# Kernel optimization log

Measured on AMD Instinct MI355X. Metric: run time of the kernel, lower is better.

Reference implementation:

```python
import jax, jax.numpy as jnp
import numpy as np

T, H, I, E, K = 16384, 2048, 1024, 8, 2  # tokens, hidden, intermediate, experts, top_k


def setup_inputs() -> dict:
    key = jax.random.key(0)
    k1, k2, k3, k4, k5 = jax.random.split(key, 5)
    hidden_states = jax.random.normal(k1, (T, H), dtype=jnp.float32)
    expert_routing_table = jax.random.randint(k2, (T, K), 0, E, dtype=jnp.int32)
    rw = jax.random.uniform(k3, (T, K), dtype=jnp.float32)
    router_weights = rw  # op consumes raw per-token gate weights
    # fused gate+up projection per expert: [E, 2I, H] (Linear-style [out, in])
    w13 = jax.random.normal(k4, (E, 2 * I, H), dtype=jnp.float32) * (1.0 / np.sqrt(H))
    # down projection per expert: [E, H, I]
    w2 = jax.random.normal(k5, (E, H, I), dtype=jnp.float32) * (1.0 / np.sqrt(I))
    return {
        "hidden_states": hidden_states,
        "expert_routing_table": expert_routing_table,
        "router_weights": router_weights,
        "w13": w13,
        "w2": w2,
    }


def reference(hidden_states, expert_routing_table, router_weights, w13, w2):
    # Faithful math of torch.ops.hpu.mixture_of_experts (silu activation):
    # for each token t and each routed expert e (top-k):
    #   g, u = split(x_t @ w13_e^T); y += router_w * ((silu(g) * u) @ w2_e^T)
    num_experts = w13.shape[0]
    out = jnp.zeros_like(hidden_states)
    for e in range(num_experts):  # small fixed expert loop
        # combine weight for expert e per token: sum over top-k slots routed to e
        coef = jnp.sum(
            jnp.where(expert_routing_table == e, router_weights, 0.0), axis=-1
        )  # [T]
        gu = hidden_states @ w13[e].T            # [T, 2I]
        g, u = jnp.split(gu, 2, axis=-1)         # SwiGLU halves
        act = jax.nn.silu(g) * u                 # [T, I]
        out = out + coef[:, None] * (act @ w2[e].T)  # [T, H]
    return out
```

## Files before the change

kernel.cpp:

```cpp
#include <hip/hip_runtime.h>
#include <hip/hip_bf16.h>
#include <stdint.h>

#define TOKS 16384
#define HDIM 2048
#define IDIM 1024
#define NEXP 8
#define TOPK 2
#define NPAIR (TOKS*TOPK)

typedef __attribute__((ext_vector_type(4))) float f32x4;
typedef __attribute__((ext_vector_type(8))) __bf16 bf16x8;
typedef __attribute__((ext_vector_type(8))) unsigned short u16x8;

#define GLOAD_LDS16(gp, lp) \
  __builtin_amdgcn_global_load_lds((const __attribute__((address_space(1))) void*)(gp), \
                                   (__attribute__((address_space(3))) void*)(lp), 16, 0, 0)

#define LGKM_WAITN(n) asm volatile("s_waitcnt lgkmcnt(" #n ")" ::: "memory")
#define VM_WAITN(n)   asm volatile("s_waitcnt vmcnt(" #n ")" ::: "memory")
#define SBAR0()       __builtin_amdgcn_sched_barrier(0)

__device__ __forceinline__ unsigned short f2bf(float f) {
  unsigned int u = __float_as_uint(f);
  u += 0x7FFF + ((u >> 16) & 1);
  return (unsigned short)(u >> 16);
}
__device__ __forceinline__ float bf2f(unsigned short h) {
  return __uint_as_float(((unsigned int)h) << 16);
}

#define W13_N8 (NEXP * 2 * IDIM * HDIM / 8)
#define W2_N8  (NEXP * HDIM * IDIM / 8)
#define X_N8   (TOKS * HDIM / 8)
__global__ __launch_bounds__(256) void cvt_all(const float* __restrict__ w13,
                                               const float* __restrict__ w2,
                                               const float* __restrict__ x,
                                               unsigned short* __restrict__ w13b,
                                               unsigned short* __restrict__ w2b,
                                               unsigned short* __restrict__ xb) {
  int i = blockIdx.x * 256 + threadIdx.x;
  const float* s; unsigned short* d; int j;
  if (i < W13_N8)              { s = w13; d = w13b; j = i; }
  else if (i < W13_N8 + W2_N8) { s = w2;  d = w2b;  j = i - W13_N8; }
  else                         { s = x;   d = xb;   j = i - W13_N8 - W2_N8; }
  const float4* sp = (const float4*)s + (size_t)j * 2;
  float4 a = sp[0], b = sp[1];
  u16x8 o;
  o[0] = f2bf(a.x); o[1] = f2bf(a.y); o[2] = f2bf(a.z); o[3] = f2bf(a.w);
  o[4] = f2bf(b.x); o[5] = f2bf(b.y); o[6] = f2bf(b.z); o[7] = f2bf(b.w);
  *((u16x8*)d + j) = o;
}

__global__ void route_count(const int* __restrict__ ert, int* __restrict__ ctrl) {
  int p = blockIdx.x * 256 + threadIdx.x;
  if (p < NPAIR) atomicAdd(&ctrl[ert[p]], 1);
}

__global__ void route_scan(int* __restrict__ ctrl) {
  if (blockIdx.x == 0 && threadIdx.x == 0) {
    int off = 0;
    for (int e = 0; e < NEXP; ++e) { ctrl[8 + e] = off; ctrl[16 + e] = off; off += ctrl[e]; }
    int toff = 0;
    for (int e = 0; e < NEXP; ++e) { ctrl[24 + e] = toff; toff += (ctrl[e] + 255) >> 8; }
    ctrl[32] = toff;
  }
}

__global__ void route_scatter(const int* __restrict__ ert, const float* __restrict__ rw,
                              int* __restrict__ ctrl, int* __restrict__ porig,
                              float* __restrict__ pcoef, int* __restrict__ pinv) {
  int p = blockIdx.x * 256 + threadIdx.x;
  if (p < NPAIR) {
    int e = ert[p];
    int pos = atomicAdd(&ctrl[16 + e], 1);
    porig[pos] = p;
    pcoef[pos] = rw[p];
    pinv[p]    = pos;
  }
}


#define RD_SET(lb, A0v, A1v, B0v, B1v) do {                                          \
  _Pragma("unroll") for (int mi = 0; mi < 4; ++mi) {                                 \
    int r_ = wr * 128 + mi * 16 + l15;                                               \
    A0v[mi] = *(const bf16x8*)((lb) + r_ * 64 + ((l16 ^ ((r_ >> 1) & 3)) << 4)); }   \
  _Pragma("unroll") for (int ni = 0; ni < 2; ++ni) {                                 \
    int nb_ = wc * 64 + ni * 16 + l15;                                               \
    B0v[ni] = *(const bf16x8*)((lb) + 16384 + nb_ * 64 + ((l16 ^ ((nb_ >> 1) & 3)) << 4)); } \
  _Pragma("unroll") for (int ni = 0; ni < 2; ++ni) {                                 \
    int nb_ = wc * 64 + 32 + ni * 16 + l15;                                          \
    B1v[ni] = *(const bf16x8*)((lb) + 16384 + nb_ * 64 + ((l16 ^ ((nb_ >> 1) & 3)) << 4)); } \
  _Pragma("unroll") for (int mi = 0; mi < 4; ++mi) {                                 \
    int r_ = wr * 128 + 64 + mi * 16 + l15;                                          \
    A1v[mi] = *(const bf16x8*)((lb) + r_ * 64 + ((l16 ^ ((r_ >> 1) & 3)) << 4)); }   \
} while (0)

#define MMQ(qm, qn, Av, Bv) do {                                                     \
  __builtin_amdgcn_s_setprio(1);                                                     \
  _Pragma("unroll") for (int mi = 0; mi < 4; ++mi)                                   \
    _Pragma("unroll") for (int ni = 0; ni < 2; ++ni)                                 \
      acc[qm][qn][mi][ni] = __builtin_amdgcn_mfma_f32_16x16x32_bf16(                 \
          Av[mi], Bv[ni], acc[qm][qn][mi][ni], 0, 0, 0);                             \
  __builtin_amdgcn_s_setprio(0);                                                     \
} while (0)

#define ITER(i, cA0, cA1, cB0, cB1, nA0, nA1, nB0, nB1) do {                         \
  LGKM_WAITN(6);                                                                     \
  MMQ(0, 0, cA0, cB0);                                                               \
  LGKM_WAITN(4);                                                                     \
  MMQ(0, 1, cA0, cB1);                                                               \
  LGKM_WAITN(0);                                                                     \
  MMQ(1, 0, cA1, cB0);                                                               \
  if ((i) < NT - 1) {                                                                \
    VM_WAITN(0);                                                                     \
    __builtin_amdgcn_s_barrier();                                                    \
    SBAR0();                                                                         \
    if ((i) + 2 < NT) STAGE((i) + 2);                                                \
    RD_SET(lds + (((i) + 1) & 1) * 32768, nA0, nA1, nB0, nB1);                       \
    SBAR0();                                                                         \
  }                                                                                  \
  MMQ(1, 1, cA1, cB1);                                                               \
} while (0)

#define TILE_MAP()                                                                   \
  const int x_ = bid & 7, k_ = bid >> 3;                                             \
  const int cb = k_ & 7;                                                             \
  const int tile = ((k_ >> 3) << 3) + x_;

__global__ __launch_bounds__(512, 2) void gemm1(const unsigned short* __restrict__ xb,
                                                const unsigned short* __restrict__ w13b,
                                                const int* __restrict__ ctrl,
                                                const int* __restrict__ porig,
                                                unsigned short* __restrict__ actb) {
  __shared__ __align__(16) char lds[65536];
  const int bid  = blockIdx.x;
  TILE_MAP();
  if (tile >= ctrl[32]) return;
  int e = 7;
  #pragma unroll
  for (int k = 7; k >= 1; --k) if (tile < ctrl[24 + k]) e = k - 1;
  const int rb   = tile - ctrl[24 + e];
  const int Ne   = ctrl[e];
  const int base = ctrl[8 + e];
  const int row0 = rb * 256;
  const int c0   = cb * 128;
  const int tid  = threadIdx.x;
  const int wid  = tid >> 6;
  const int lane = tid & 63;
  const int wr   = wid >> 2;
  const int wc   = wid & 3;
  const int l15  = lane & 15;
  const int l16  = lane >> 4;
  const int NT   = HDIM / 32;

  const unsigned short *gA0, *gA1, *gB0, *gB1;
  {
    int rl = wid * 16 + (lane >> 2);
    int r0 = rl, r1 = 128 + rl;
    int c80 = (lane & 3) ^ ((r0 >> 1) & 3);
    int c81 = (lane & 3) ^ ((r1 >> 1) & 3);
    int rr0 = row0 + r0; if (rr0 > Ne - 1) rr0 = Ne - 1;
    int rr1 = row0 + r1; if (rr1 > Ne - 1) rr1 = Ne - 1;
    gA0 = xb + (size_t)(porig[base + rr0] >> 1) * HDIM + c80 * 8;
    gA1 = xb + (size_t)(porig[base + rr1] >> 1) * HDIM + c81 * 8;
    int g0 = ((r0 & 32) ? IDIM : 0) + c0 + ((r0 >> 6) << 5) + (r0 & 31);
    int g1 = ((r1 & 32) ? IDIM : 0) + c0 + ((r1 >> 6) << 5) + (r1 & 31);
    gB0 = w13b + ((size_t)e * (2 * IDIM) + g0) * HDIM + c80 * 8;
    gB1 = w13b + ((size_t)e * (2 * IDIM) + g1) * HDIM + c81 * 8;
  }

  f32x4 acc[2][2][4][2];
  #pragma unroll
  for (int qm = 0; qm < 2; ++qm)
    #pragma unroll
    for (int qn = 0; qn < 2; ++qn)
      #pragma unroll
      for (int mi = 0; mi < 4; ++mi)
        #pragma unroll
        for (int ni = 0; ni < 2; ++ni) acc[qm][qn][mi][ni] = (f32x4)(0.0f);

  auto STAGE = [&](int kt) {
    char* d = lds + (kt & 1) * 32768 + wid * 1024;
    GLOAD_LDS16(gA0 + kt * 32, d);
    GLOAD_LDS16(gA1 + kt * 32, d + 8192);
    GLOAD_LDS16(gB0 + kt * 32, d + 16384);
    GLOAD_LDS16(gB1 + kt * 32, d + 24576);
  };

  bf16x8 A0a[4], A1a[4], B0a[2], B1a[2];
  bf16x8 A0b[4], A1b[4], B0b[2], B1b[2];

  STAGE(0); STAGE(1);
  VM_WAITN(4);
  __builtin_amdgcn_s_barrier();
  SBAR0();
  RD_SET(lds, A0a, A1a, B0a, B1a);
  SBAR0();

  for (int i = 0; i < NT; i += 2) {
    ITER(i,     A0a, A1a, B0a, B1a, A0b, A1b, B0b, B1b);
    ITER(i + 1, A0b, A1b, B0b, B1b, A0a, A1a, B0a, B1a);
  }

  #pragma unroll
  for (int qm = 0; qm < 2; ++qm)
    #pragma unroll
    for (int mi = 0; mi < 4; ++mi)
      #pragma unroll
      for (int jj = 0; jj < 4; ++jj) {
        int r = wr * 128 + qm * 64 + mi * 16 + l16 * 4 + jj;
        int rr = row0 + r;
        if (rr < Ne) {
          #pragma unroll
          for (int ni = 0; ni < 2; ++ni) {
            float g = acc[qm][0][mi][ni][jj];
            float u = acc[qm][1][mi][ni][jj];
            float a = g / (1.0f + __expf(-g)) * u;
            actb[(size_t)(base + rr) * IDIM + (c0 + wc * 32 + ni * 16 + l15)] = f2bf(a);
          }
        }
      }
}

__global__ __launch_bounds__(512, 2) void gemm2(const unsigned short* __restrict__ actb,
                                                const unsigned short* __restrict__ w2b,
                                                const int* __restrict__ ctrl,
                                                const float* __restrict__ pcoef,
                                                unsigned short* __restrict__ yb) {
  __shared__ __align__(16) char lds[65536];
  const int bid  = blockIdx.x;
  TILE_MAP();
  if (tile >= ctrl[32]) return;
  int e = 7;
  #pragma unroll
  for (int k = 7; k >= 1; --k) if (tile < ctrl[24 + k]) e = k - 1;
  const int rb   = tile - ctrl[24 + e];
  const int Ne   = ctrl[e];
  const int base = ctrl[8 + e];
  const int row0 = rb * 256;
  const int n0   = cb * 256;
  const int tid  = threadIdx.x;
  const int wid  = tid >> 6;
  const int lane = tid & 63;
  const int wr   = wid >> 2;
  const int wc   = wid & 3;
  const int l15  = lane & 15;
  const int l16  = lane >> 4;
  const int NT   = IDIM / 32;

  const unsigned short *gA0, *gA1, *gB0, *gB1;
  {
    int rl = wid * 16 + (lane >> 2);
    int r0 = rl, r1 = 128 + rl;
    int c80 = (lane & 3) ^ ((r0 >> 1) & 3);
    int c81 = (lane & 3) ^ ((r1 >> 1) & 3);
    int rr0 = row0 + r0; if (rr0 > Ne - 1) rr0 = Ne - 1;
    int rr1 = row0 + r1; if (rr1 > Ne - 1) rr1 = Ne - 1;
    gA0 = actb + (size_t)(base + rr0) * IDIM + c80 * 8;
    gA1 = actb + (size_t)(base + rr1) * IDIM + c81 * 8;
    gB0 = w2b + ((size_t)e * HDIM + n0 + r0) * IDIM + c80 * 8;
    gB1 = w2b + ((size_t)e * HDIM + n0 + r1) * IDIM + c81 * 8;
  }

  f32x4 acc[2][2][4][2];
  #pragma unroll
  for (int qm = 0; qm < 2; ++qm)
    #pragma unroll
    for (int qn = 0; qn < 2; ++qn)
      #pragma unroll
      for (int mi = 0; mi < 4; ++mi)
        #pragma unroll
        for (int ni = 0; ni < 2; ++ni) acc[qm][qn][mi][ni] = (f32x4)(0.0f);

  auto STAGE = [&](int kt) {
    char* d = lds + (kt & 1) * 32768 + wid * 1024;
    GLOAD_LDS16(gA0 + kt * 32, d);
    GLOAD_LDS16(gA1 + kt * 32, d + 8192);
    GLOAD_LDS16(gB0 + kt * 32, d + 16384);
    GLOAD_LDS16(gB1 + kt * 32, d + 24576);
  };

  bf16x8 A0a[4], A1a[4], B0a[2], B1a[2];
  bf16x8 A0b[4], A1b[4], B0b[2], B1b[2];

  STAGE(0); STAGE(1);
  VM_WAITN(4);
  __builtin_amdgcn_s_barrier();
  SBAR0();
  RD_SET(lds, A0a, A1a, B0a, B1a);
  SBAR0();

  for (int i = 0; i < NT; i += 2) {
    ITER(i,     A0a, A1a, B0a, B1a, A0b, A1b, B0b, B1b);
    ITER(i + 1, A0b, A1b, B0b, B1b, A0a, A1a, B0a, B1a);
  }

  #pragma unroll
  for (int qm = 0; qm < 2; ++qm)
    #pragma unroll
    for (int mi = 0; mi < 4; ++mi)
      #pragma unroll
      for (int jj = 0; jj < 4; ++jj) {
        int r = wr * 128 + qm * 64 + mi * 16 + l16 * 4 + jj;
        int rr = row0 + r;
        if (rr < Ne) {
          float cf = pcoef[base + rr];
          #pragma unroll
          for (int qn = 0; qn < 2; ++qn)
            #pragma unroll
            for (int ni = 0; ni < 2; ++ni) {
              int col = n0 + wc * 64 + qn * 32 + ni * 16 + l15;
              yb[(size_t)(base + rr) * HDIM + col] = f2bf(acc[qm][qn][mi][ni][jj] * cf);
            }
        }
      }
}

__global__ __launch_bounds__(256) void reduce2(const unsigned short* __restrict__ yb,
                                               const int* __restrict__ pinv,
                                               float* __restrict__ out) {
  int i = blockIdx.x * 256 + threadIdx.x;
  int t = i >> 8;
  int g = i & 255;
  int p0 = pinv[2 * t], p1 = pinv[2 * t + 1];
  u16x8 a = *((const u16x8*)(yb + (size_t)p0 * HDIM) + g);
  u16x8 b = *((const u16x8*)(yb + (size_t)p1 * HDIM) + g);
  float4 o0, o1;
  o0.x = bf2f(a[0]) + bf2f(b[0]); o0.y = bf2f(a[1]) + bf2f(b[1]);
  o0.z = bf2f(a[2]) + bf2f(b[2]); o0.w = bf2f(a[3]) + bf2f(b[3]);
  o1.x = bf2f(a[4]) + bf2f(b[4]); o1.y = bf2f(a[5]) + bf2f(b[5]);
  o1.z = bf2f(a[6]) + bf2f(b[6]); o1.w = bf2f(a[7]) + bf2f(b[7]);
  float4* dst = (float4*)(out + (size_t)t * HDIM) + g * 2;
  dst[0] = o0; dst[1] = o1;
}

extern "C" void kernel_launch(void* const* d_in, const int* in_sizes, int n_in,
                              void* d_out, int out_size, void* d_ws, size_t ws_size,
                              hipStream_t stream) {
  const float* x   = (const float*)d_in[0];
  const int*   ert = (const int*)d_in[1];
  const float* rw  = (const float*)d_in[2];
  const float* w13 = (const float*)d_in[3];
  const float* w2  = (const float*)d_in[4];
  float* out = (float*)d_out;

  char* ws = (char*)d_ws;
  size_t off = 0;
  auto alloc = [&](size_t bytes) { char* p = ws + off; off += (bytes + 255) & ~255ULL; return p; };
  int*            ctrl  = (int*)           alloc(256);
  int*            porig = (int*)           alloc((size_t)NPAIR * 4);
  float*          pcoef = (float*)         alloc((size_t)NPAIR * 4);
  int*            pinv  = (int*)           alloc((size_t)NPAIR * 4);
  unsigned short* w2b   = (unsigned short*)alloc((size_t)NEXP * HDIM * IDIM * 2);
  unsigned short* actb  = (unsigned short*)alloc((size_t)NPAIR * IDIM * 2);
  unsigned short* w13b  = (unsigned short*)alloc((size_t)NEXP * 2 * IDIM * HDIM * 2);
  unsigned short* xb    = (unsigned short*)alloc((size_t)TOKS * HDIM * 2);
  unsigned short* yb    = w13b;

  hipMemsetAsync(ctrl, 0, 256, stream);

  cvt_all<<<(W13_N8 + W2_N8 + X_N8) / 256, 256, 0, stream>>>(w13, w2, x, w13b, w2b, xb);

  route_count  <<<NPAIR / 256, 256, 0, stream>>>(ert, ctrl);
  route_scan   <<<1, 64, 0, stream>>>(ctrl);
  route_scatter<<<NPAIR / 256, 256, 0, stream>>>(ert, rw, ctrl, porig, pcoef, pinv);

  gemm1<<<136 * 8, 512, 0, stream>>>(xb, w13b, ctrl, porig, actb);
  gemm2<<<136 * 8, 512, 0, stream>>>(actb, w2b, ctrl, pcoef, yb);
  reduce2<<<(TOKS * HDIM / 8) / 256, 256, 0, stream>>>(yb, pinv, out);
}
```

Baseline: 863.7 us.

## Shrink GEMM tiles to 256x128 and simplify pipeline to single-stage register reads

Halves the N dimension of each block tile in both expert GEMMs (256x256 to 256x128 in gemm1's gate/up pair, 256x128 in gemm2), doubling the grid to 2176 blocks and cutting LDS to 48KB. The unrolled ping-pong register double-buffering with staggered LDS waits is replaced by a simpler loop that reads all fragments, waits for LDS, then issues 16 MFMAs per wave. The aim is more blocks for load balance and occupancy, at the cost of lower arithmetic intensity per tile and less overlap of LDS reads with MFMA.

```diff
diff --git a/kernel.cpp b/kernel.cpp
--- a/kernel.cpp
+++ b/kernel.cpp
@@ -81,80 +81,72 @@
 }
 
 
-#define RD_SET(lb, A0v, A1v, B0v, B1v) do {                                          \
+#define RD8(lb) do {                                                                 \
   _Pragma("unroll") for (int mi = 0; mi < 4; ++mi) {                                 \
-    int r_ = wr * 128 + mi * 16 + l15;                                               \
-    A0v[mi] = *(const bf16x8*)((lb) + r_ * 64 + ((l16 ^ ((r_ >> 1) & 3)) << 4)); }   \
-  _Pragma("unroll") for (int ni = 0; ni < 2; ++ni) {                                 \
+    int r_ = wr * 64 + mi * 16 + l15;                                                \
+    fA[mi] = *(const bf16x8*)((lb) + r_ * 64 + ((l16 ^ ((r_ >> 1) & 3)) << 4)); }    \
+  _Pragma("unroll") for (int ni = 0; ni < 4; ++ni) {                                 \
     int nb_ = wc * 64 + ni * 16 + l15;                                               \
-    B0v[ni] = *(const bf16x8*)((lb) + 16384 + nb_ * 64 + ((l16 ^ ((nb_ >> 1) & 3)) << 4)); } \
-  _Pragma("unroll") for (int ni = 0; ni < 2; ++ni) {                                 \
-    int nb_ = wc * 64 + 32 + ni * 16 + l15;                                          \
-    B1v[ni] = *(const bf16x8*)((lb) + 16384 + nb_ * 64 + ((l16 ^ ((nb_ >> 1) & 3)) << 4)); } \
-  _Pragma("unroll") for (int mi = 0; mi < 4; ++mi) {                                 \
-    int r_ = wr * 128 + 64 + mi * 16 + l15;                                          \
-    A1v[mi] = *(const bf16x8*)((lb) + r_ * 64 + ((l16 ^ ((r_ >> 1) & 3)) << 4)); }   \
+    fB[ni] = *(const bf16x8*)((lb) + 16384 + nb_ * 64 + ((l16 ^ ((nb_ >> 1) & 3)) << 4)); } \
 } while (0)
 
-#define MMQ(qm, qn, Av, Bv) do {                                                     \
+#define MFMA16() do {                                                                \
   __builtin_amdgcn_s_setprio(1);                                                     \
   _Pragma("unroll") for (int mi = 0; mi < 4; ++mi)                                   \
-    _Pragma("unroll") for (int ni = 0; ni < 2; ++ni)                                 \
-      acc[qm][qn][mi][ni] = __builtin_amdgcn_mfma_f32_16x16x32_bf16(                 \
-          Av[mi], Bv[ni], acc[qm][qn][mi][ni], 0, 0, 0);                             \
+    _Pragma("unroll") for (int ni = 0; ni < 4; ++ni)                                 \
+      acc[mi][ni] = __builtin_amdgcn_mfma_f32_16x16x32_bf16(                         \
+          fA[mi], fB[ni], acc[mi][ni], 0, 0, 0);                                     \
   __builtin_amdgcn_s_setprio(0);                                                     \
 } while (0)
 
-#define ITER(i, cA0, cA1, cB0, cB1, nA0, nA1, nB0, nB1) do {                         \
-  LGKM_WAITN(6);                                                                     \
-  MMQ(0, 0, cA0, cB0);                                                               \
-  LGKM_WAITN(4);                                                                     \
-  MMQ(0, 1, cA0, cB1);                                                               \
-  LGKM_WAITN(0);                                                                     \
-  MMQ(1, 0, cA1, cB0);                                                               \
-  if ((i) < NT - 1) {                                                                \
-    VM_WAITN(0);                                                                     \
-    __builtin_amdgcn_s_barrier();                                                    \
-    SBAR0();                                                                         \
-    if ((i) + 2 < NT) STAGE((i) + 2);                                                \
-    RD_SET(lds + (((i) + 1) & 1) * 32768, nA0, nA1, nB0, nB1);                       \
-    SBAR0();                                                                         \
+#define GEMM_LOOP() do {                                                             \
+  STAGE(0);                                                                          \
+  VM_WAITN(0);                                                                       \
+  __builtin_amdgcn_s_barrier();                                                      \
+  for (int i = 0; i < NT; ++i) {                                                     \
+    if (i + 1 < NT) STAGE(i + 1);                                                    \
+    const char* lb_ = lds + (i & 1) * 24576;                                         \
+    RD8(lb_);                                                                        \
+    LGKM_WAITN(0); SBAR0();                                                          \
+    MFMA16();                                                                        \
+    if (i + 1 < NT) {                                                                \
+      VM_WAITN(0);                                                                   \
+      __builtin_amdgcn_s_barrier();                                                  \
+    }                                                                                \
   }                                                                                  \
-  MMQ(1, 1, cA1, cB1);                                                               \
 } while (0)
 
-#define TILE_MAP()                                                                   \
+#define TILE_MAP16()                                                                 \
   const int x_ = bid & 7, k_ = bid >> 3;                                             \
-  const int cb = k_ & 7;                                                             \
-  const int tile = ((k_ >> 3) << 3) + x_;
+  const int cb = k_ & 15;                                                            \
+  const int tile = ((k_ >> 4) << 3) + x_;
 
 __global__ __launch_bounds__(512, 2) void gemm1(const unsigned short* __restrict__ xb,
                                                 const unsigned short* __restrict__ w13b,
                                                 const int* __restrict__ ctrl,
                                                 const int* __restrict__ porig,
                                                 unsigned short* __restrict__ actb) {
-  __shared__ __align__(16) char lds[65536];
+  __shared__ __align__(16) char lds[49152];
   const int bid  = blockIdx.x;
-  TILE_MAP();
+  TILE_MAP16();
   if (tile >= ctrl[32]) return;
   int e = 7;
   #pragma unroll
   for (int k = 7; k >= 1; --k) if (tile < ctrl[24 + k]) e = k - 1;
-  const int rb   = tile - ctrl[24 + e];
   const int Ne   = ctrl[e];
   const int base = ctrl[8 + e];
-  const int row0 = rb * 256;
-  const int c0   = cb * 128;
+  const int row0 = (tile - ctrl[24 + e]) * 256;
+  const int c0   = cb * 64;
   const int tid  = threadIdx.x;
   const int wid  = tid >> 6;
   const int lane = tid & 63;
-  const int wr   = wid >> 2;
-  const int wc   = wid & 3;
+  const int wr   = wid >> 1;
+  const int wc   = wid & 1;
   const int l15  = lane & 15;
   const int l16  = lane >> 4;
   const int NT   = HDIM / 32;
 
-  const unsigned short *gA0, *gA1, *gB0, *gB1;
+  const unsigned short *gA0, *gA1, *gB0;
   {
     int rl = wid * 16 + (lane >> 2);
     int r0 = rl, r1 = 128 + rl;
@@ -164,63 +156,43 @@
     int rr1 = row0 + r1; if (rr1 > Ne - 1) rr1 = Ne - 1;
     gA0 = xb + (size_t)(porig[base + rr0] >> 1) * HDIM + c80 * 8;
     gA1 = xb + (size_t)(porig[base + rr1] >> 1) * HDIM + c81 * 8;
-    int g0 = ((r0 & 32) ? IDIM : 0) + c0 + ((r0 >> 6) << 5) + (r0 & 31);
-    int g1 = ((r1 & 32) ? IDIM : 0) + c0 + ((r1 >> 6) << 5) + (r1 & 31);
-    gB0 = w13b + ((size_t)e * (2 * IDIM) + g0) * HDIM + c80 * 8;
-    gB1 = w13b + ((size_t)e * (2 * IDIM) + g1) * HDIM + c81 * 8;
+    int n  = rl & 63;
+    int gr = ((n & 32) ? IDIM : 0) + c0 + ((rl >> 6) << 5) + (n & 31);
+    gB0 = w13b + ((size_t)e * (2 * IDIM) + gr) * HDIM + c80 * 8;
   }
 
-  f32x4 acc[2][2][4][2];
-  #pragma unroll
-  for (int qm = 0; qm < 2; ++qm)
+  f32x4 acc[4][4];
+  #pragma unroll
+  for (int mi = 0; mi < 4; ++mi)
     #pragma unroll
-    for (int qn = 0; qn < 2; ++qn)
-      #pragma unroll
-      for (int mi = 0; mi < 4; ++mi)
-        #pragma unroll
-        for (int ni = 0; ni < 2; ++ni) acc[qm][qn][mi][ni] = (f32x4)(0.0f);
+    for (int ni = 0; ni < 4; ++ni) acc[mi][ni] = (f32x4)(0.0f);
 
   auto STAGE = [&](int kt) {
-    char* d = lds + (kt & 1) * 32768 + wid * 1024;
+    char* d = lds + (kt & 1) * 24576 + wid * 1024;
     GLOAD_LDS16(gA0 + kt * 32, d);
     GLOAD_LDS16(gA1 + kt * 32, d + 8192);
     GLOAD_LDS16(gB0 + kt * 32, d + 16384);
-    GLOAD_LDS16(gB1 + kt * 32, d + 24576);
   };
 
-  bf16x8 A0a[4], A1a[4], B0a[2], B1a[2];
-  bf16x8 A0b[4], A1b[4], B0b[2], B1b[2];
-
-  STAGE(0); STAGE(1);
-  VM_WAITN(4);
-  __builtin_amdgcn_s_barrier();
-  SBAR0();
-  RD_SET(lds, A0a, A1a, B0a, B1a);
-  SBAR0();
-
-  for (int i = 0; i < NT; i += 2) {
-    ITER(i,     A0a, A1a, B0a, B1a, A0b, A1b, B0b, B1b);
-    ITER(i + 1, A0b, A1b, B0b, B1b, A0a, A1a, B0a, B1a);
-  }
-
-  #pragma unroll
-  for (int qm = 0; qm < 2; ++qm)
+  bf16x8 fA[4], fB[4];
+  GEMM_LOOP();
+
+  #pragma unroll
+  for (int mi = 0; mi < 4; ++mi)
     #pragma unroll
-    for (int mi = 0; mi < 4; ++mi)
-      #pragma unroll
-      for (int jj = 0; jj < 4; ++jj) {
-        int r = wr * 128 + qm * 64 + mi * 16 + l16 * 4 + jj;
-        int rr = row0 + r;
-        if (rr < Ne) {
-          #pragma unroll
-          for (int ni = 0; ni < 2; ++ni) {
-            float g = acc[qm][0][mi][ni][jj];
-            float u = acc[qm][1][mi][ni][jj];
-            float a = g / (1.0f + __expf(-g)) * u;
-            actb[(size_t)(base + rr) * IDIM + (c0 + wc * 32 + ni * 16 + l15)] = f2bf(a);
-          }
+    for (int jj = 0; jj < 4; ++jj) {
+      int r  = wr * 64 + mi * 16 + l16 * 4 + jj;
+      int rr = row0 + r;
+      if (rr < Ne) {
+        #pragma unroll
+        for (int ni = 0; ni < 2; ++ni) {
+          float g = acc[mi][ni][jj];
+          float u = acc[mi][ni + 2][jj];
+          float a = g / (1.0f + __expf(-g)) * u;
+          actb[(size_t)(base + rr) * IDIM + (c0 + wc * 32 + ni * 16 + l15)] = f2bf(a);
         }
       }
+    }
 }
 
 __global__ __launch_bounds__(512, 2) void gemm2(const unsigned short* __restrict__ actb,
@@ -228,28 +200,27 @@
                                                 const int* __restrict__ ctrl,
                                                 const float* __restrict__ pcoef,
                                                 unsigned short* __restrict__ yb) {
-  __shared__ __align__(16) char lds[65536];
+  __shared__ __align__(16) char lds[49152];
   const int bid  = blockIdx.x;
-  TILE_MAP();
+  TILE_MAP16();
   if (tile >= ctrl[32]) return;
   int e = 7;
   #pragma unroll
   for (int k = 7; k >= 1; --k) if (tile < ctrl[24 + k]) e = k - 1;
-  const int rb   = tile - ctrl[24 + e];
   const int Ne   = ctrl[e];
   const int base = ctrl[8 + e];
-  const int row0 = rb * 256;
-  const int n0   = cb * 256;
+  const int row0 = (tile - ctrl[24 + e]) * 256;
+  const int n0   = cb * 128;
   const int tid  = threadIdx.x;
   const int wid  = tid >> 6;
   const int lane = tid & 63;
-  const int wr   = wid >> 2;
-  const int wc   = wid & 3;
+  const int wr   = wid >> 1;
+  const int wc   = wid & 1;
   const int l15  = lane & 15;
   const int l16  = lane >> 4;
   const int NT   = IDIM / 32;
 
-  const unsigned short *gA0, *gA1, *gB0, *gB1;
+  const unsigned short *gA0, *gA1, *gB0;
   {
     int rl = wid * 16 + (lane >> 2);
     int r0 = rl, r1 = 128 + rl;
@@ -259,62 +230,40 @@
     int rr1 = row0 + r1; if (rr1 > Ne - 1) rr1 = Ne - 1;
     gA0 = actb + (size_t)(base + rr0) * IDIM + c80 * 8;
     gA1 = actb + (size_t)(base + rr1) * IDIM + c81 * 8;
-    gB0 = w2b + ((size_t)e * HDIM + n0 + r0) * IDIM + c80 * 8;
-    gB1 = w2b + ((size_t)e * HDIM + n0 + r1) * IDIM + c81 * 8;
+    gB0 = w2b + ((size_t)e * HDIM + n0 + rl) * IDIM + c80 * 8;
   }
 
-  f32x4 acc[2][2][4][2];
-  #pragma unroll
-  for (int qm = 0; qm < 2; ++qm)
+  f32x4 acc[4][4];
+  #pragma unroll
+  for (int mi = 0; mi < 4; ++mi)
     #pragma unroll
-    for (int qn = 0; qn < 2; ++qn)
-      #pragma unroll
-      for (int mi = 0; mi < 4; ++mi)
-        #pragma unroll
-        for (int ni = 0; ni < 2; ++ni) acc[qm][qn][mi][ni] = (f32x4)(0.0f);
+    for (int ni = 0; ni < 4; ++ni) acc[mi][ni] = (f32x4)(0.0f);
 
   auto STAGE = [&](int kt) {
-    char* d = lds + (kt & 1) * 32768 + wid * 1024;
+    char* d = lds + (kt & 1) * 24576 + wid * 1024;
     GLOAD_LDS16(gA0 + kt * 32, d);
     GLOAD_LDS16(gA1 + kt * 32, d + 8192);
     GLOAD_LDS16(gB0 + kt * 32, d + 16384);
-    GLOAD_LDS16(gB1 + kt * 32, d + 24576);
   };
 
-  bf16x8 A0a[4], A1a[4], B0a[2], B1a[2];
-  bf16x8 A0b[4], A1b[4], B0b[2], B1b[2];
-
-  STAGE(0); STAGE(1);
-  VM_WAITN(4);
-  __builtin_amdgcn_s_barrier();
-  SBAR0();
-  RD_SET(lds, A0a, A1a, B0a, B1a);
-  SBAR0();
-
-  for (int i = 0; i < NT; i += 2) {
-    ITER(i,     A0a, A1a, B0a, B1a, A0b, A1b, B0b, B1b);
-    ITER(i + 1, A0b, A1b, B0b, B1b, A0a, A1a, B0a, B1a);
-  }
-
-  #pragma unroll
-  for (int qm = 0; qm < 2; ++qm)
+  bf16x8 fA[4], fB[4];
+  GEMM_LOOP();
+
+  #pragma unroll
+  for (int mi = 0; mi < 4; ++mi)
     #pragma unroll
-    for (int mi = 0; mi < 4; ++mi)
-      #pragma unroll
-      for (int jj = 0; jj < 4; ++jj) {
-        int r = wr * 128 + qm * 64 + mi * 16 + l16 * 4 + jj;
-        int rr = row0 + r;
-        if (rr < Ne) {
-          float cf = pcoef[base + rr];
-          #pragma unroll
-          for (int qn = 0; qn < 2; ++qn)
-            #pragma unroll
-            for (int ni = 0; ni < 2; ++ni) {
-              int col = n0 + wc * 64 + qn * 32 + ni * 16 + l15;
-              yb[(size_t)(base + rr) * HDIM + col] = f2bf(acc[qm][qn][mi][ni][jj] * cf);
-            }
+    for (int jj = 0; jj < 4; ++jj) {
+      int r  = wr * 64 + mi * 16 + l16 * 4 + jj;
+      int rr = row0 + r;
+      if (rr < Ne) {
+        float cf = pcoef[base + rr];
+        #pragma unroll
+        for (int ni = 0; ni < 4; ++ni) {
+          int col = n0 + wc * 64 + ni * 16 + l15;
+          yb[(size_t)(base + rr) * HDIM + col] = f2bf(acc[mi][ni][jj] * cf);
         }
       }
+    }
 }
 
 __global__ __launch_bounds__(256) void reduce2(const unsigned short* __restrict__ yb,
@@ -366,7 +315,7 @@
   route_scan   <<<1, 64, 0, stream>>>(ctrl);
   route_scatter<<<NPAIR / 256, 256, 0, stream>>>(ert, rw, ctrl, porig, pcoef, pinv);
 
-  gemm1<<<136 * 8, 512, 0, stream>>>(xb, w13b, ctrl, porig, actb);
-  gemm2<<<136 * 8, 512, 0, stream>>>(actb, w2b, ctrl, pcoef, yb);
+  gemm1<<<2176, 512, 0, stream>>>(xb, w13b, ctrl, porig, actb);
+  gemm2<<<2176, 512, 0, stream>>>(actb, w2b, ctrl, pcoef, yb);
   reduce2<<<(TOKS * HDIM / 8) / 256, 256, 0, stream>>>(yb, pinv, out);
 }
```

After: 847.5 us. No clear change (-1.9%).

## Load B operand directly from global into registers and deepen A LDS pipeline

Applied to the files above, without the earlier changes.

Both MoE GEMM kernels stop staging the weight (B) tiles through LDS. Each wave now loads its B fragments straight from global memory into registers one k-step ahead. The freed LDS is used to turn the A-tile double buffer into a 4-stage ring prefetched three steps ahead, with vmcnt waits adjusted to match. The aim is to cut LDS traffic and bank pressure and to deepen latency hiding. The cost is more uncoalesced global loads per wave, duplicate B loads across the two wave rows, and more register pressure.

```diff
diff --git a/kernel.cpp b/kernel.cpp
--- a/kernel.cpp
+++ b/kernel.cpp
@@ -81,19 +81,20 @@
 }
 
 
-#define RD_SET(lb, A0v, A1v, B0v, B1v) do {                                          \
+#define RD_A(lb, A0v, A1v) do {                                                      \
   _Pragma("unroll") for (int mi = 0; mi < 4; ++mi) {                                 \
     int r_ = wr * 128 + mi * 16 + l15;                                               \
     A0v[mi] = *(const bf16x8*)((lb) + r_ * 64 + ((l16 ^ ((r_ >> 1) & 3)) << 4)); }   \
-  _Pragma("unroll") for (int ni = 0; ni < 2; ++ni) {                                 \
-    int nb_ = wc * 64 + ni * 16 + l15;                                               \
-    B0v[ni] = *(const bf16x8*)((lb) + 16384 + nb_ * 64 + ((l16 ^ ((nb_ >> 1) & 3)) << 4)); } \
-  _Pragma("unroll") for (int ni = 0; ni < 2; ++ni) {                                 \
-    int nb_ = wc * 64 + 32 + ni * 16 + l15;                                          \
-    B1v[ni] = *(const bf16x8*)((lb) + 16384 + nb_ * 64 + ((l16 ^ ((nb_ >> 1) & 3)) << 4)); } \
   _Pragma("unroll") for (int mi = 0; mi < 4; ++mi) {                                 \
     int r_ = wr * 128 + 64 + mi * 16 + l15;                                          \
     A1v[mi] = *(const bf16x8*)((lb) + r_ * 64 + ((l16 ^ ((r_ >> 1) & 3)) << 4)); }   \
+} while (0)
+
+#define LOADB(i, B) do {                                                             \
+  B[0][0] = *(const bf16x8*)(gB00 + (size_t)(i) * 32);                               \
+  B[0][1] = *(const bf16x8*)(gB01 + (size_t)(i) * 32);                               \
+  B[1][0] = *(const bf16x8*)(gB10 + (size_t)(i) * 32);                               \
+  B[1][1] = *(const bf16x8*)(gB11 + (size_t)(i) * 32);                               \
 } while (0)
 
 #define MMQ(qm, qn, Av, Bv) do {                                                     \
@@ -105,22 +106,39 @@
   __builtin_amdgcn_s_setprio(0);                                                     \
 } while (0)
 
-#define ITER(i, cA0, cA1, cB0, cB1, nA0, nA1, nB0, nB1) do {                         \
-  LGKM_WAITN(6);                                                                     \
-  MMQ(0, 0, cA0, cB0);                                                               \
-  LGKM_WAITN(4);                                                                     \
-  MMQ(0, 1, cA0, cB1);                                                               \
-  LGKM_WAITN(0);                                                                     \
-  MMQ(1, 0, cA1, cB0);                                                               \
+#define ITER(i, cA0, cA1, cB, nA0, nA1, nB) do {                                     \
+  if ((i) + 3 < NT) STAGE((i) + 3);                                                  \
+  if ((i) + 1 < NT) LOADB((i) + 1, nB);                                              \
+  if ((i) < NT - 3)      { VM_WAITN(6); }                                            \
+  else if ((i) < NT - 1) { VM_WAITN(4); }                                            \
+  else                   { VM_WAITN(0); }                                            \
+  SBAR0();                                                                           \
+  LGKM_WAITN(4); SBAR0();                                                            \
+  MMQ(0, 0, cA0, (cB)[0]);                                                           \
+  MMQ(0, 1, cA0, (cB)[1]);                                                           \
+  LGKM_WAITN(0); SBAR0();                                                            \
+  MMQ(1, 0, cA1, (cB)[0]);                                                           \
   if ((i) < NT - 1) {                                                                \
-    VM_WAITN(0);                                                                     \
     __builtin_amdgcn_s_barrier();                                                    \
     SBAR0();                                                                         \
-    if ((i) + 2 < NT) STAGE((i) + 2);                                                \
-    RD_SET(lds + (((i) + 1) & 1) * 32768, nA0, nA1, nB0, nB1);                       \
+    RD_A(lds + (((i) + 1) & 3) * 16384, nA0, nA1);                                   \
     SBAR0();                                                                         \
   }                                                                                  \
-  MMQ(1, 1, cA1, cB1);                                                               \
+  MMQ(1, 1, cA1, (cB)[1]);                                                           \
+} while (0)
+
+#define GEMM_BODY() do {                                                             \
+  STAGE(0); STAGE(1); STAGE(2);                                                      \
+  LOADB(0, Bc);                                                                      \
+  VM_WAITN(8);                                    \
+  __builtin_amdgcn_s_barrier();                                                      \
+  SBAR0();                                                                           \
+  RD_A(lds, A0a, A1a);                                                               \
+  SBAR0();                                                                           \
+  for (int i = 0; i < NT; i += 2) {                                                  \
+    ITER(i,     A0a, A1a, Bc, A0b, A1b, Bn);                                         \
+    ITER(i + 1, A0b, A1b, Bn, A0a, A1a, Bc);                                         \
+  }                                                                                  \
 } while (0)
 
 #define TILE_MAP()                                                                   \
@@ -140,10 +158,9 @@
   int e = 7;
   #pragma unroll
   for (int k = 7; k >= 1; --k) if (tile < ctrl[24 + k]) e = k - 1;
-  const int rb   = tile - ctrl[24 + e];
   const int Ne   = ctrl[e];
   const int base = ctrl[8 + e];
-  const int row0 = rb * 256;
+  const int row0 = (tile - ctrl[24 + e]) * 256;
   const int c0   = cb * 128;
   const int tid  = threadIdx.x;
   const int wid  = tid >> 6;
@@ -154,7 +171,7 @@
   const int l16  = lane >> 4;
   const int NT   = HDIM / 32;
 
-  const unsigned short *gA0, *gA1, *gB0, *gB1;
+  const unsigned short *gA0, *gA1;
   {
     int rl = wid * 16 + (lane >> 2);
     int r0 = rl, r1 = 128 + rl;
@@ -164,10 +181,14 @@
     int rr1 = row0 + r1; if (rr1 > Ne - 1) rr1 = Ne - 1;
     gA0 = xb + (size_t)(porig[base + rr0] >> 1) * HDIM + c80 * 8;
     gA1 = xb + (size_t)(porig[base + rr1] >> 1) * HDIM + c81 * 8;
-    int g0 = ((r0 & 32) ? IDIM : 0) + c0 + ((r0 >> 6) << 5) + (r0 & 31);
-    int g1 = ((r1 & 32) ? IDIM : 0) + c0 + ((r1 >> 6) << 5) + (r1 & 31);
-    gB0 = w13b + ((size_t)e * (2 * IDIM) + g0) * HDIM + c80 * 8;
-    gB1 = w13b + ((size_t)e * (2 * IDIM) + g1) * HDIM + c81 * 8;
+  }
+  const unsigned short *gB00, *gB01, *gB10, *gB11;
+  {
+    int colb = c0 + wc * 32 + l15;
+    gB00 = w13b + ((size_t)e * 2 * IDIM + colb)             * HDIM + l16 * 8;
+    gB01 = w13b + ((size_t)e * 2 * IDIM + colb + 16)        * HDIM + l16 * 8;
+    gB10 = w13b + ((size_t)e * 2 * IDIM + IDIM + colb)      * HDIM + l16 * 8;
+    gB11 = w13b + ((size_t)e * 2 * IDIM + IDIM + colb + 16) * HDIM + l16 * 8;
   }
 
   f32x4 acc[2][2][4][2];
@@ -181,27 +202,15 @@
         for (int ni = 0; ni < 2; ++ni) acc[qm][qn][mi][ni] = (f32x4)(0.0f);
 
   auto STAGE = [&](int kt) {
-    char* d = lds + (kt & 1) * 32768 + wid * 1024;
+    char* d = lds + (kt & 3) * 16384 + wid * 1024;
     GLOAD_LDS16(gA0 + kt * 32, d);
     GLOAD_LDS16(gA1 + kt * 32, d + 8192);
-    GLOAD_LDS16(gB0 + kt * 32, d + 16384);
-    GLOAD_LDS16(gB1 + kt * 32, d + 24576);
   };
 
-  bf16x8 A0a[4], A1a[4], B0a[2], B1a[2];
-  bf16x8 A0b[4], A1b[4], B0b[2], B1b[2];
-
-  STAGE(0); STAGE(1);
-  VM_WAITN(4);
-  __builtin_amdgcn_s_barrier();
-  SBAR0();
-  RD_SET(lds, A0a, A1a, B0a, B1a);
-  SBAR0();
-
-  for (int i = 0; i < NT; i += 2) {
-    ITER(i,     A0a, A1a, B0a, B1a, A0b, A1b, B0b, B1b);
-    ITER(i + 1, A0b, A1b, B0b, B1b, A0a, A1a, B0a, B1a);
-  }
+  bf16x8 A0a[4], A1a[4], A0b[4], A1b[4];
+  bf16x8 Bc[2][2], Bn[2][2];
+
+  GEMM_BODY();
 
   #pragma unroll
   for (int qm = 0; qm < 2; ++qm)
@@ -235,10 +244,9 @@
   int e = 7;
   #pragma unroll
   for (int k = 7; k >= 1; --k) if (tile < ctrl[24 + k]) e = k - 1;
-  const int rb   = tile - ctrl[24 + e];
   const int Ne   = ctrl[e];
   const int base = ctrl[8 + e];
-  const int row0 = rb * 256;
+  const int row0 = (tile - ctrl[24 + e]) * 256;
   const int n0   = cb * 256;
   const int tid  = threadIdx.x;
   const int wid  = tid >> 6;
@@ -249,7 +257,7 @@
   const int l16  = lane >> 4;
   const int NT   = IDIM / 32;
 
-  const unsigned short *gA0, *gA1, *gB0, *gB1;
+  const unsigned short *gA0, *gA1;
   {
     int rl = wid * 16 + (lane >> 2);
     int r0 = rl, r1 = 128 + rl;
@@ -259,8 +267,14 @@
     int rr1 = row0 + r1; if (rr1 > Ne - 1) rr1 = Ne - 1;
     gA0 = actb + (size_t)(base + rr0) * IDIM + c80 * 8;
     gA1 = actb + (size_t)(base + rr1) * IDIM + c81 * 8;
-    gB0 = w2b + ((size_t)e * HDIM + n0 + r0) * IDIM + c80 * 8;
-    gB1 = w2b + ((size_t)e * HDIM + n0 + r1) * IDIM + c81 * 8;
+  }
+  const unsigned short *gB00, *gB01, *gB10, *gB11;
+  {
+    int rowb = n0 + wc * 64 + l15;
+    gB00 = w2b + ((size_t)e * HDIM + rowb)      * IDIM + l16 * 8;
+    gB01 = w2b + ((size_t)e * HDIM + rowb + 16) * IDIM + l16 * 8;
+    gB10 = w2b + ((size_t)e * HDIM + rowb + 32) * IDIM + l16 * 8;
+    gB11 = w2b + ((size_t)e * HDIM + rowb + 48) * IDIM + l16 * 8;
   }
 
   f32x4 acc[2][2][4][2];
@@ -274,27 +288,15 @@
         for (int ni = 0; ni < 2; ++ni) acc[qm][qn][mi][ni] = (f32x4)(0.0f);
 
   auto STAGE = [&](int kt) {
-    char* d = lds + (kt & 1) * 32768 + wid * 1024;
+    char* d = lds + (kt & 3) * 16384 + wid * 1024;
     GLOAD_LDS16(gA0 + kt * 32, d);
     GLOAD_LDS16(gA1 + kt * 32, d + 8192);
-    GLOAD_LDS16(gB0 + kt * 32, d + 16384);
-    GLOAD_LDS16(gB1 + kt * 32, d + 24576);
   };
 
-  bf16x8 A0a[4], A1a[4], B0a[2], B1a[2];
-  bf16x8 A0b[4], A1b[4], B0b[2], B1b[2];
-
-  STAGE(0); STAGE(1);
-  VM_WAITN(4);
-  __builtin_amdgcn_s_barrier();
-  SBAR0();
-  RD_SET(lds, A0a, A1a, B0a, B1a);
-  SBAR0();
-
-  for (int i = 0; i < NT; i += 2) {
-    ITER(i,     A0a, A1a, B0a, B1a, A0b, A1b, B0b, B1b);
-    ITER(i + 1, A0b, A1b, B0b, B1b, A0a, A1a, B0a, B1a);
-  }
+  bf16x8 A0a[4], A1a[4], A0b[4], A1b[4];
+  bf16x8 Bc[2][2], Bn[2][2];
+
+  GEMM_BODY();
 
   #pragma unroll
   for (int qm = 0; qm < 2; ++qm)
```

Measured after the change: 1.118 ms. 1.29x slower.
